# Performance work log

Measured on AMD Instinct MI355X. Metric: run time of the kernel, lower is better.

Reference implementation:

```python
import jax, jax.numpy as jnp
import numpy as np

INPUT_SIZE = 9
HIDDEN = 50
OUTPUT = 1


def setup_inputs() -> dict:
    key = jax.random.key(0)
    ks = jax.random.split(key, 7)
    B, T = 4096, 512
    s_ih = 1.0 / np.sqrt(HIDDEN)
    inp = {
        "x": jax.random.normal(ks[0], (B, T, INPUT_SIZE), dtype=jnp.float32),
        # PyTorch LSTM params, gate order [i, f, g, o]
        "w_ih": jax.random.uniform(ks[1], (4 * HIDDEN, INPUT_SIZE), minval=-s_ih, maxval=s_ih, dtype=jnp.float32),
        "w_hh": jax.random.uniform(ks[2], (4 * HIDDEN, HIDDEN), minval=-s_ih, maxval=s_ih, dtype=jnp.float32),
        "b_ih": jax.random.uniform(ks[3], (4 * HIDDEN,), minval=-s_ih, maxval=s_ih, dtype=jnp.float32),
        "b_hh": jax.random.uniform(ks[4], (4 * HIDDEN,), minval=-s_ih, maxval=s_ih, dtype=jnp.float32),
        "fc_w": jax.random.uniform(ks[5], (OUTPUT, HIDDEN), minval=-s_ih, maxval=s_ih, dtype=jnp.float32),
        "fc_b": jax.random.uniform(ks[6], (OUTPUT,), minval=-s_ih, maxval=s_ih, dtype=jnp.float32),
    }
    return inp


def _lstm_last_h(x, w_ih, w_hh, b_ih, b_hh):
    B, T, _ = x.shape
    H = w_hh.shape[1]
    # Precompute input-side gate pre-activations for all timesteps: [T, B, 4H]
    x_gates = jnp.einsum("bti,gi->tbg", x, w_ih) + (b_ih + b_hh)

    def step(carry, xg):
        h, c = carry
        gates = xg + h @ w_hh.T  # [B, 4H]
        i, f, g, o = jnp.split(gates, 4, axis=-1)
        i = jax.nn.sigmoid(i)
        f = jax.nn.sigmoid(f)
        g = jnp.tanh(g)
        o = jax.nn.sigmoid(o)
        c = f * c + i * g
        h = o * jnp.tanh(c)
        return (h, c), None

    h0 = jnp.zeros((B, H), dtype=x.dtype)
    c0 = jnp.zeros((B, H), dtype=x.dtype)
    (h_last, _), _ = jax.lax.scan(step, (h0, c0), x_gates)
    return h_last


def reference(x, w_ih, w_hh, b_ih, b_hh, fc_w, fc_b):
    h_last = _lstm_last_h(x, w_ih, w_hh, b_ih, b_hh)  # [B, H]
    return h_last @ fc_w.T + fc_b  # [B, 1]
```

## Files before the change

### kernel.cpp

```cpp
#include <hip/hip_runtime.h>
#include <hip/hip_bf16.h>

#define TT    512
#define ISZ   9
#define HH    50
#define NB    16
#define NWAVE 16
#define NTH   (NWAVE * 64)
#define KDIM  64

typedef _Float16 f16x8_t __attribute__((ext_vector_type(8)));
typedef float    f32x4_t __attribute__((ext_vector_type(4)));

#define L2E    1.44269504088896340736f
#define TWOL2E 2.88539008177792681472f

#define BAR() asm volatile("s_waitcnt lgkmcnt(0)\n\ts_barrier" ::: "memory")

__device__ __forceinline__ unsigned short f16h(float v) {
  _Float16 b = (_Float16)v;
  return __builtin_bit_cast(unsigned short, b);
}
__device__ __forceinline__ float sg_exp2(float z) { return __builtin_amdgcn_exp2f(z); }
__device__ __forceinline__ float rcp_f(float z)   { return __builtin_amdgcn_rcpf(z); }

__global__ __launch_bounds__(NTH, 1) void lstm_mfma(
    const float* __restrict__ x,
    const float* __restrict__ w_ih,
    const float* __restrict__ w_hh,
    const float* __restrict__ b_ih,
    const float* __restrict__ b_hh,
    const float* __restrict__ fc_w,
    const float* __restrict__ fc_b,
    float* __restrict__ out) {
  __shared__ __align__(16) unsigned short hbuf[2][NB * KDIM];
  __shared__ float redbuf[NWAVE][NB];

  const int tid = threadIdx.x;
  const int w   = tid >> 6;
  const int l   = tid & 63;
  const int lb  = l & 15;
  const int kq  = l >> 4;
  const int b0  = blockIdx.x * NB;
  const bool cw = (w < 13);

  for (int i = tid; i < (2 * NB * KDIM) / 2; i += NTH)
    reinterpret_cast<unsigned*>(hbuf)[i] = 0u;

  const int xt = tid - 13 * 64;
  const bool xact = (xt >= 0 && xt < NB * ISZ);
  const int xb = xact ? (xt / ISZ) : 0;
  const int xi = xact ? (xt - xb * ISZ) : 0;
  __syncthreads();
  if (xact) {
    float xv = x[(size_t)(b0 + xb) * (TT * ISZ) + xi];
    *(unsigned short*)((char*)hbuf[0] + (((xb << 7) + ((50 + xi) << 1)) ^ ((xb & 7) << 4))) = f16h(xv);
  }

  f16x8_t afrag[2];
  {
    const int rp   = w * 16 + lb;
    const int jA   = rp >> 2;
    const int gA   = rp & 3;
    const int rowA = gA * HH + jA;
    const bool liveA = cw && (jA < HH);
    const float scA = (gA == 2) ? TWOL2E : (-L2E);
#pragma unroll
    for (int ks = 0; ks < 2; ++ks) {
#pragma unroll
      for (int e = 0; e < 8; ++e) {
        const int K = ks * 32 + kq * 8 + e;
        float v = 0.0f;
        if (liveA) {
          if (K < HH)            v = w_hh[rowA * HH + K] * scA;
          else if (K < HH + ISZ) v = w_ih[rowA * ISZ + (K - HH)] * scA;
        }
        afrag[ks][e] = (_Float16)v;
      }
    }
  }

  const int j0 = w * 4 + kq;
  const bool live0 = cw && (j0 < HH);
  f32x4_t bias0 = {0.f, 0.f, 0.f, 0.f};
  if (live0) {
#pragma unroll
    for (int r = 0; r < 4; ++r) {
      const float sc = (r == 2) ? TWOL2E : (-L2E);
      bias0[r] = (b_ih[r * HH + j0] + b_hh[r * HH + j0]) * sc;
    }
  }
  const f32x4_t zeroC = {0.f, 0.f, 0.f, 0.f};

  char* const base = (char*)hbuf[0];
  const int swzb = (lb & 7) << 4;
  const int rd0 = ((lb << 7) + 0  + (kq << 4)) ^ swzb;
  const int rd1 = ((lb << 7) + 64 + (kq << 4)) ^ swzb;
  const int j0c = (j0 < HH) ? j0 : (j0 + 9);
  const int wo0 = (((lb << 7) + (j0c << 1)) ^ swzb);
  const int xwo = (((xb << 7) + ((50 + xi) << 1)) ^ ((xb & 7) << 4));

  const float* xp = x + (size_t)(b0 + xb) * (TT * ISZ) + xi;
  float csc = 0.0f, h0 = 0.0f;
  float xv_n = 0.0f;
  if (xact) xv_n = xp[ISZ];
  xp += 2 * ISZ;

#define STEP(T, CUR, NXT)                                                        \
  if (cw) {                                                                      \
    BAR();                                                                       \
    f16x8_t bb0 = *(const f16x8_t*)(base + rd0 + (CUR));                         \
    f16x8_t bb1 = *(const f16x8_t*)(base + rd1 + (CUR));                         \
    f32x4_t accA = __builtin_amdgcn_mfma_f32_16x16x32_f16(afrag[0], bb0, bias0, 0,0,0); \
    f32x4_t accB = __builtin_amdgcn_mfma_f32_16x16x32_f16(afrag[1], bb1, zeroC, 0,0,0); \
    const float z0 = accA[0] + accB[0];                                          \
    const float z1 = accA[1] + accB[1];                                          \
    const float z2 = accA[2] + accB[2];                                          \
    const float z3 = accA[3] + accB[3];                                          \
    const float pi = sg_exp2(z0);                                    \
    const float pf = sg_exp2(z1);                                    \
    const float eg = sg_exp2(z2);                                    \
    const float po = sg_exp2(z3);                                    \
    const float A1 = 1.0f + pi, A2 = 1.0f + eg, A3 = 1.0f + pf;                  \
    const float P  = A1 * A2;                                                    \
    const float R  = rcp_f(P * A3);                                              \
    const float t1 = fmaf(P, csc, (eg - 1.0f) * TWOL2E * A3);                    \
    csc = t1 * R;                                             \
    const float ec = sg_exp2(csc);                                               \
    const float r2 = rcp_f((1.0f + po) * (1.0f + ec));                           \
    h0 = (ec - 1.0f) * r2;                                                       \
    *(unsigned short*)(base + wo0 + (NXT)) = f16h(h0);                           \
  } else {                                                                       \
    float xv_new = 0.0f;                                                         \
    if (xact && (T) + 2 < TT) xv_new = *xp;                                      \
    xp += ISZ;                                                                   \
    BAR();                                                                       \
    if (xact && (T) + 1 < TT) *(unsigned short*)(base + xwo + (NXT)) = f16h(xv_n); \
    xv_n = xv_new;                                                               \
  }

  for (int t2 = 0; t2 < TT; t2 += 2) {
    STEP(t2,     0x000, 0x800);
    STEP(t2 + 1, 0x800, 0x000);
  }
#undef STEP

  float p = live0 ? h0 * fc_w[j0] : 0.0f;
  p += __shfl_xor(p, 16);
  p += __shfl_xor(p, 32);
  if (l < NB) redbuf[w][l] = p;
  __syncthreads();
  if (tid < NB) {
    float a = fc_b[0];
#pragma unroll
    for (int ww = 0; ww < NWAVE; ++ww) a += redbuf[ww][tid];
    out[b0 + tid] = a;
  }
}

extern "C" void kernel_launch(void* const* d_in, const int* in_sizes, int n_in,
                              void* d_out, int out_size, void* d_ws, size_t ws_size,
                              hipStream_t stream) {
  const float* x    = (const float*)d_in[0];
  const float* w_ih = (const float*)d_in[1];
  const float* w_hh = (const float*)d_in[2];
  const float* b_ih = (const float*)d_in[3];
  const float* b_hh = (const float*)d_in[4];
  const float* fc_w = (const float*)d_in[5];
  const float* fc_b = (const float*)d_in[6];
  float* out = (float*)d_out;
  const int Btot = in_sizes[0] / (TT * ISZ);
  dim3 grid(Btot / NB), block(NTH);
  hipLaunchKernelGGL(lstm_mfma, grid, block, 0, stream,
                     x, w_ih, w_hh, b_ih, b_hh, fc_w, fc_b, out);
}
```

Before: 192.7 us.

## Halve batch per block and give each compute wave two gate tiles

Each block now handles 8 batch rows with 8 waves instead of 16 rows with 16 waves, so two blocks can share a CU (launch bounds raised to 4). Each compute wave now computes two 16-row gate tiles against the same 8-column hidden state, chaining the K halves in the MFMA accumulator. The upper 8 lanes take the second tile's result through a lane shuffle, and the input x is staged by a single wave. The aim is smaller per-block barriers and two independent recurrences per CU that can hide each other's latency. The cost is that half of each MFMA's batch columns go unused, and every step adds shuffles and a longer dependent MFMA chain.

```diff
diff --git a/kernel.cpp b/kernel.cpp
--- a/kernel.cpp
+++ b/kernel.cpp
@@ -4,8 +4,8 @@
 #define TT    512
 #define ISZ   9
 #define HH    50
-#define NB    16
-#define NWAVE 16
+#define NB    8
+#define NWAVE 8
 #define NTH   (NWAVE * 64)
 #define KDIM  64
 
@@ -24,7 +24,7 @@
 __device__ __forceinline__ float sg_exp2(float z) { return __builtin_amdgcn_exp2f(z); }
 __device__ __forceinline__ float rcp_f(float z)   { return __builtin_amdgcn_rcpf(z); }
 
-__global__ __launch_bounds__(NTH, 1) void lstm_mfma(
+__global__ __launch_bounds__(NTH, 4) void lstm_mfma(
     const float* __restrict__ x,
     const float* __restrict__ w_ih,
     const float* __restrict__ w_hh,
@@ -41,29 +41,40 @@
   const int l   = tid & 63;
   const int lb  = l & 15;
   const int kq  = l >> 4;
+  const int bsel = lb & 7;
+  const bool upper = (lb >= 8);
   const int b0  = blockIdx.x * NB;
-  const bool cw = (w < 13);
+  const bool cw = (w < 7);
 
   for (int i = tid; i < (2 * NB * KDIM) / 2; i += NTH)
     reinterpret_cast<unsigned*>(hbuf)[i] = 0u;
 
-  const int xt = tid - 13 * 64;
-  const bool xact = (xt >= 0 && xt < NB * ISZ);
-  const int xb = xact ? (xt / ISZ) : 0;
-  const int xi = xact ? (xt - xb * ISZ) : 0;
+  const bool sw = (w == 7);
+  const int e1 = l, e2 = 64 + l;
+  const bool s2 = sw && (l < 8);
+  const int b1 = e1 / ISZ, i1 = e1 - b1 * ISZ;
+  const int b2 = e2 / ISZ, i2 = e2 - b2 * ISZ;
+  const int xwo1 = ((b1 << 7) + ((50 + i1) << 1)) ^ (b1 << 4);
+  const int xwo2 = ((b2 << 7) + ((50 + i2) << 1)) ^ (b2 << 4);
+  const float* xp1 = x + (size_t)(b0 + b1) * (TT * ISZ) + i1;
+  const float* xp2 = x + (size_t)(b0 + (b2 & 7)) * (TT * ISZ) + i2;
   __syncthreads();
-  if (xact) {
-    float xv = x[(size_t)(b0 + xb) * (TT * ISZ) + xi];
-    *(unsigned short*)((char*)hbuf[0] + (((xb << 7) + ((50 + xi) << 1)) ^ ((xb & 7) << 4))) = f16h(xv);
-  }
-
-  f16x8_t afrag[2];
-  {
-    const int rp   = w * 16 + lb;
-    const int jA   = rp >> 2;
+  if (sw) {
+    *(unsigned short*)((char*)hbuf[0] + xwo1) = f16h(*xp1);
+    if (s2) *(unsigned short*)((char*)hbuf[0] + xwo2) = f16h(*xp2);
+  }
+
+  const int tA = (w < 6) ? (2 * w)     : 12;
+  const int tB = (w < 6) ? (2 * w + 1) : 12;
+  f16x8_t afragA[2], afragB[2];
+#pragma unroll
+  for (int tt = 0; tt < 2; ++tt) {
+    const int tile = tt ? tB : tA;
+    const int rp   = tile * 16 + lb;
+    const int jA_  = rp >> 2;
     const int gA   = rp & 3;
-    const int rowA = gA * HH + jA;
-    const bool liveA = cw && (jA < HH);
+    const int rowA = gA * HH + jA_;
+    const bool liveA = cw && (jA_ < HH);
     const float scA = (gA == 2) ? TWOL2E : (-L2E);
 #pragma unroll
     for (int ks = 0; ks < 2; ++ks) {
@@ -75,48 +86,55 @@
           if (K < HH)            v = w_hh[rowA * HH + K] * scA;
           else if (K < HH + ISZ) v = w_ih[rowA * ISZ + (K - HH)] * scA;
         }
-        afrag[ks][e] = (_Float16)v;
+        if (tt) afragB[ks][e] = (_Float16)v; else afragA[ks][e] = (_Float16)v;
       }
     }
   }
 
-  const int j0 = w * 4 + kq;
-  const bool live0 = cw && (j0 < HH);
-  f32x4_t bias0 = {0.f, 0.f, 0.f, 0.f};
-  if (live0) {
-#pragma unroll
-    for (int r = 0; r < 4; ++r) {
-      const float sc = (r == 2) ? TWOL2E : (-L2E);
-      bias0[r] = (b_ih[r * HH + j0] + b_hh[r * HH + j0]) * sc;
-    }
-  }
-  const f32x4_t zeroC = {0.f, 0.f, 0.f, 0.f};
+  const int jA = tA * 4 + kq;
+  const int jB = tB * 4 + kq;
+  const bool liveA0 = cw && (jA < HH);
+  const bool liveB0 = cw && (w < 6);
+  f32x4_t biasA = {0.f, 0.f, 0.f, 0.f};
+  f32x4_t biasB = {0.f, 0.f, 0.f, 0.f};
+#pragma unroll
+  for (int r = 0; r < 4; ++r) {
+    const float sc = (r == 2) ? TWOL2E : (-L2E);
+    if (liveA0) biasA[r] = (b_ih[r * HH + jA] + b_hh[r * HH + jA]) * sc;
+    if (liveB0) biasB[r] = (b_ih[r * HH + jB] + b_hh[r * HH + jB]) * sc;
+  }
 
   char* const base = (char*)hbuf[0];
-  const int swzb = (lb & 7) << 4;
-  const int rd0 = ((lb << 7) + 0  + (kq << 4)) ^ swzb;
-  const int rd1 = ((lb << 7) + 64 + (kq << 4)) ^ swzb;
-  const int j0c = (j0 < HH) ? j0 : (j0 + 9);
-  const int wo0 = (((lb << 7) + (j0c << 1)) ^ swzb);
-  const int xwo = (((xb << 7) + ((50 + xi) << 1)) ^ ((xb & 7) << 4));
-
-  const float* xp = x + (size_t)(b0 + xb) * (TT * ISZ) + xi;
+  const int swzb = bsel << 4;
+  const int rd0 = ((bsel << 7) + 0  + (kq << 4)) ^ swzb;
+  const int rd1 = ((bsel << 7) + 64 + (kq << 4)) ^ swzb;
+  const int kA = (jA < HH) ? jA : 63;
+  const int kB = (w < 6) ? jB : (59 + kq);
+  const int ksel = upper ? kB : kA;
+  const int woS = (((bsel << 7) + (ksel << 1)) ^ swzb);
+
   float csc = 0.0f, h0 = 0.0f;
-  float xv_n = 0.0f;
-  if (xact) xv_n = xp[ISZ];
-  xp += 2 * ISZ;
+  float xv1 = 0.0f, xv2 = 0.0f;
+  if (sw) { xv1 = xp1[ISZ]; xp1 += 2 * ISZ; }
+  if (s2) { xv2 = xp2[ISZ]; xp2 += 2 * ISZ; }
 
 #define STEP(T, CUR, NXT)                                                        \
   if (cw) {                                                                      \
     BAR();                                                                       \
     f16x8_t bb0 = *(const f16x8_t*)(base + rd0 + (CUR));                         \
     f16x8_t bb1 = *(const f16x8_t*)(base + rd1 + (CUR));                         \
-    f32x4_t accA = __builtin_amdgcn_mfma_f32_16x16x32_f16(afrag[0], bb0, bias0, 0,0,0); \
-    f32x4_t accB = __builtin_amdgcn_mfma_f32_16x16x32_f16(afrag[1], bb1, zeroC, 0,0,0); \
-    const float z0 = accA[0] + accB[0];                                          \
-    const float z1 = accA[1] + accB[1];                                          \
-    const float z2 = accA[2] + accB[2];                                          \
-    const float z3 = accA[3] + accB[3];                                          \
+    f32x4_t accA = __builtin_amdgcn_mfma_f32_16x16x32_f16(afragA[0], bb0, biasA, 0,0,0); \
+    f32x4_t accB = __builtin_amdgcn_mfma_f32_16x16x32_f16(afragB[0], bb0, biasB, 0,0,0); \
+    accA = __builtin_amdgcn_mfma_f32_16x16x32_f16(afragA[1], bb1, accA, 0,0,0);  \
+    accB = __builtin_amdgcn_mfma_f32_16x16x32_f16(afragB[1], bb1, accB, 0,0,0);  \
+    const float s0 = __shfl_xor(accB[0], 8);                                     \
+    const float s1 = __shfl_xor(accB[1], 8);                                     \
+    const float s2v = __shfl_xor(accB[2], 8);                                    \
+    const float s3 = __shfl_xor(accB[3], 8);                                     \
+    const float z0 = upper ? s0 : accA[0];                                       \
+    const float z1 = upper ? s1 : accA[1];                                       \
+    const float z2 = upper ? s2v : accA[2];                                      \
+    const float z3 = upper ? s3 : accA[3];                                       \
     const float pi = sg_exp2(z0);                                    \
     const float pf = sg_exp2(z1);                                    \
     const float eg = sg_exp2(z2);                                    \
@@ -129,23 +147,32 @@
     const float ec = sg_exp2(csc);                                               \
     const float r2 = rcp_f((1.0f + po) * (1.0f + ec));                           \
     h0 = (ec - 1.0f) * r2;                                                       \
-    *(unsigned short*)(base + wo0 + (NXT)) = f16h(h0);                           \
+    *(unsigned short*)(base + woS + (NXT)) = f16h(h0);                           \
   } else {                                                                       \
-    float xv_new = 0.0f;                                                         \
-    if (xact && (T) + 2 < TT) xv_new = *xp;                                      \
-    xp += ISZ;                                                                   \
+    float xn1 = 0.0f, xn2 = 0.0f;                                                \
+    if (sw && (T) + 2 < TT) { xn1 = *xp1; if (s2) xn2 = *xp2; }                  \
+    if (sw) xp1 += ISZ;                                                          \
+    if (s2) xp2 += ISZ;                                                          \
     BAR();                                                                       \
-    if (xact && (T) + 1 < TT) *(unsigned short*)(base + xwo + (NXT)) = f16h(xv_n); \
-    xv_n = xv_new;                                                               \
+    if (sw && (T) + 1 < TT) {                                                    \
+      *(unsigned short*)(base + xwo1 + (NXT)) = f16h(xv1);                       \
+      if (s2) *(unsigned short*)(base + xwo2 + (NXT)) = f16h(xv2);               \
+    }                                                                            \
+    xv1 = xn1; xv2 = xn2;                                                        \
   }
 
   for (int t2 = 0; t2 < TT; t2 += 2) {
-    STEP(t2,     0x000, 0x800);
-    STEP(t2 + 1, 0x800, 0x000);
+    STEP(t2,     0x000, 0x400);
+    STEP(t2 + 1, 0x400, 0x000);
   }
 #undef STEP
 
-  float p = live0 ? h0 * fc_w[j0] : 0.0f;
+  float p = 0.0f;
+  if (cw) {
+    if (!upper) { if (jA < HH) p = h0 * fc_w[jA]; }
+    else if (w < 6) p = h0 * fc_w[jB];
+  }
+  p += __shfl_xor(p, 8);
   p += __shfl_xor(p, 16);
   p += __shfl_xor(p, 32);
   if (l < NB) redbuf[w][l] = p;
```

Result: slower. 232.9 us (+20.9%).
